# Kernel tuning notes

Hardware: AMD Instinct MI355X
Metric: run time of the kernel (lower is better)

Reference implementation:

```python
import jax, jax.numpy as jnp
import numpy as np

HEADS = 8
DIM_HEAD = 64
SCALE = DIM_HEAD ** -0.5
QUERY_DIM = 512
CTX_DIM = 64
INNER = HEADS * DIM_HEAD  # 512
GATE_HID = 32


def setup_inputs() -> dict:
    key = jax.random.key(0)
    ks = jax.random.split(key, 11)
    B, N, M = 4, 2048, 2048
    s = lambda fan: 1.0 / np.sqrt(fan)
    return {
        "x": jax.random.normal(ks[0], (B, N, QUERY_DIM), dtype=jnp.float32),
        "context": jax.random.normal(ks[1], (B, M, CTX_DIM), dtype=jnp.float32),
        "Wq": jax.random.normal(ks[2], (QUERY_DIM, INNER), dtype=jnp.float32) * s(QUERY_DIM),
        "Wk": jax.random.normal(ks[3], (CTX_DIM, INNER), dtype=jnp.float32) * s(CTX_DIM),
        "Wv": jax.random.normal(ks[4], (CTX_DIM, INNER), dtype=jnp.float32) * s(CTX_DIM),
        "W1": jax.random.normal(ks[5], (CTX_DIM, GATE_HID), dtype=jnp.float32) * s(CTX_DIM),
        "b1": jnp.zeros((GATE_HID,), dtype=jnp.float32),
        "W2": jax.random.normal(ks[6], (GATE_HID, 1), dtype=jnp.float32) * s(GATE_HID),
        "b2": jnp.zeros((1,), dtype=jnp.float32),
        "Wo": jax.random.normal(ks[7], (INNER, QUERY_DIM), dtype=jnp.float32) * s(INNER),
        "bo": jnp.zeros((QUERY_DIM,), dtype=jnp.float32),
    }


def reference(x, context, Wq, Wk, Wv, W1, b1, W2, b2, Wo, bo):
    B, N, _ = x.shape
    M = context.shape[1]
    # visual reliability gate: sigmoid(relu(ctx @ W1 + b1) @ W2 + b2) -> [B, M, 1]
    gate = jax.nn.sigmoid(jax.nn.relu(context @ W1 + b1) @ W2 + b2)
    ctx = context * gate
    # projections
    q = (x @ Wq).reshape(B, N, HEADS, DIM_HEAD).transpose(0, 2, 1, 3)    # [B,H,N,D]
    k = (ctx @ Wk).reshape(B, M, HEADS, DIM_HEAD).transpose(0, 2, 1, 3)  # [B,H,M,D]
    v = (ctx @ Wv).reshape(B, M, HEADS, DIM_HEAD).transpose(0, 2, 1, 3)  # [B,H,M,D]
    # scaled dot-product attention (full score matrix, as in source)
    sim = jnp.einsum('bhid,bhjd->bhij', q, k) * SCALE
    attn = jax.nn.softmax(sim, axis=-1)
    out = jnp.einsum('bhij,bhjd->bhid', attn, v)
    out = out.transpose(0, 2, 1, 3).reshape(B, N, INNER)
    return out @ Wo + bo
```

## Files before the change

### kernel.cpp

```cpp
#include <hip/hip_runtime.h>

typedef unsigned short u16;
typedef unsigned int u32;
using frag16 = __attribute__((ext_vector_type(8))) short;
using facc   = __attribute__((ext_vector_type(4))) float;
using facc16 = __attribute__((ext_vector_type(16))) float;

#define DEV static __device__ __forceinline__

DEV u16 f2bf(float f) {
  union { float f; unsigned u; } v; v.f = f;
  unsigned r = v.u + 0x7fffu + ((v.u >> 16) & 1u);
  return (u16)(r >> 16);
}
DEV unsigned fbits(float f) {
  union { float f; unsigned u; } v; v.f = f;
  return v.u;
}
DEV unsigned pkbf(float lo, float hi) {
  return __builtin_amdgcn_perm(fbits(hi) + 0x8000u, fbits(lo) + 0x8000u, 0x07060302u);
}
DEV void gld16(const u16* g, u16* l) {
  __builtin_amdgcn_global_load_lds(
      (__attribute__((address_space(1))) unsigned int*)(g),
      (__attribute__((address_space(3))) unsigned int*)(l), 16, 0, 0);
}

__global__ __launch_bounds__(256) void prep_gate_kernel(const float4* __restrict__ x,
    const float* __restrict__ Wq, const float* __restrict__ Wk,
    const float* __restrict__ Wv, const float* __restrict__ Wo,
    const float* __restrict__ ctx, const float* __restrict__ W1,
    const float* __restrict__ b1, const float* __restrict__ W2,
    const float* __restrict__ b2,
    u16* __restrict__ xb, u16* __restrict__ WqT, u16* __restrict__ WkT,
    u16* __restrict__ WvT, u16* __restrict__ WoT, u16* __restrict__ gctx) {
  int bid = blockIdx.x;
  if (bid < 4096) {
    int id = bid * 256 + threadIdx.x;
    float4 v = x[id];
    ushort4 o;
    o.x = f2bf(v.x); o.y = f2bf(v.y); o.z = f2bf(v.z); o.w = f2bf(v.w);
    *(ushort4*)(xb + (size_t)id * 4) = o;
  } else if (bid < 6400) {
    int id = (bid - 4096) * 256 + threadIdx.x;
    const float* W; u16* WT; int K, idx;
    if (id < 262144)      { W = Wq; WT = WqT; K = 512; idx = id; }
    else if (id < 294912) { W = Wk; WT = WkT; K = 64;  idx = id - 262144; }
    else if (id < 327680) { W = Wv; WT = WvT; K = 64;  idx = id - 294912; }
    else                  { W = Wo; WT = WoT; K = 512; idx = id - 327680; }
    int n = idx / K, k = idx - n * K;
    WT[idx] = f2bf(W[k * 512 + n]);
  } else {
    int wave = threadIdx.x >> 6, lane = threadIdx.x & 63;
    int row = (bid - 6400) * 4 + wave;
    __shared__ float sc[4][64];
    float cv = ctx[(size_t)row * 64 + lane];
    sc[wave][lane] = cv;
    __syncthreads();
    float h = 0.f;
    if (lane < 32) {
      h = b1[lane];
      #pragma unroll
      for (int i = 0; i < 64; ++i) h += sc[wave][i] * W1[i * 32 + lane];
      h = fmaxf(h, 0.f) * W2[lane];
    }
    #pragma unroll
    for (int off = 32; off; off >>= 1) h += __shfl_xor(h, off);
    float g = 1.f / (1.f + __expf(-(h + b2[0])));
    gctx[(size_t)row * 64 + lane] = f2bf(cv * g);
  }
}

template<int MODE>
DEV void gemm128_body(const u16* __restrict__ A, const u16* __restrict__ BT,
                      void* __restrict__ Cp, const float* __restrict__ bias,
                      int m0, int n0, float scale,
                      u16* As0, u16* As1, u16* Bs0, u16* Bs1) {
  const int K = 512, N = 512;
  const int lane = threadIdx.x & 63, wave = threadIdx.x >> 6;
  const int quad = lane >> 4, l16 = lane & 15;
  const int wr = wave >> 1, wc = wave & 1;

  const u16* gA = A + (size_t)(m0 + wave * 32 + (lane >> 2)) * K + (lane & 3) * 8;
  const u16* gB = BT + (size_t)(n0 + wave * 16 + (lane >> 2)) * K + (lane & 3) * 8;

  facc acc[4][2] = {};

  for (int k0 = 0; k0 < K; k0 += 64) {
    if (k0) __syncthreads();
    gld16(gA + k0,           As0 + wave * 1024);
    gld16(gA + 16 * K + k0,  As0 + wave * 1024 + 512);
    gld16(gA + k0 + 32,          As1 + wave * 1024);
    gld16(gA + 16 * K + k0 + 32, As1 + wave * 1024 + 512);
    gld16(gB + k0,      Bs0 + wave * 512);
    gld16(gB + k0 + 32, Bs1 + wave * 512);
    __syncthreads();

    #pragma unroll
    for (int hh = 0; hh < 2; ++hh) {
      const u16* Ah = hh ? As1 : As0;
      const u16* Bh = hh ? Bs1 : Bs0;
      frag16 af[4], bf[2];
      #pragma unroll
      for (int rt = 0; rt < 4; ++rt)
        af[rt] = *(const frag16*)(Ah + (wr * 64 + rt * 16 + l16) * 32 + quad * 8);
      #pragma unroll
      for (int ct = 0; ct < 2; ++ct)
        bf[ct] = *(const frag16*)(Bh + (wc * 32 + ct * 16 + l16) * 32 + quad * 8);
      #pragma unroll
      for (int rt = 0; rt < 4; ++rt)
        #pragma unroll
        for (int ct = 0; ct < 2; ++ct)
          acc[rt][ct] = __builtin_amdgcn_mfma_f32_16x16x32_bf16(af[rt], bf[ct], acc[rt][ct], 0, 0, 0);
    }
  }

  #pragma unroll
  for (int rt = 0; rt < 4; ++rt) {
    #pragma unroll
    for (int ct = 0; ct < 2; ++ct) {
      int col = n0 + wc * 32 + ct * 16 + l16;
      int r0g = m0 + wr * 64 + rt * 16 + quad * 4;
      if (MODE == 0) {
        u16* C = (u16*)Cp;
        #pragma unroll
        for (int r = 0; r < 4; ++r)
          C[(size_t)(r0g + r) * N + col] = f2bf(acc[rt][ct][r] * scale);
      } else {
        float* C = (float*)Cp;
        float bv = bias[col];
        #pragma unroll
        for (int r = 0; r < 4; ++r)
          C[(size_t)(r0g + r) * N + col] = acc[rt][ct][r] + bv;
      }
    }
  }
}

__global__ __launch_bounds__(256) void proj_kernel(const u16* __restrict__ xb,
    const u16* __restrict__ WqT, u16* __restrict__ qb,
    const u16* __restrict__ gctx, const u16* __restrict__ BkT,
    const u16* __restrict__ BvT, u16* __restrict__ Kp, u16* __restrict__ Vp) {
  __shared__ __align__(16) u16 As0[128 * 32], As1[128 * 32];
  __shared__ __align__(16) u16 Bs0[64 * 32], Bs1[64 * 32];
  int bid = blockIdx.x;
  if (bid < 512) {
    int n0 = (bid & 7) * 64, m0 = (bid >> 3) * 128;
    gemm128_body<0>(xb, WqT, qb, nullptr, m0, n0,
                    0.125f * 1.4426950408889634f, As0, As1, Bs0, Bs1);
    return;
  }
  bid -= 512;
  const int Kd = 64;
  int lane = threadIdx.x & 63, wave = threadIdx.x >> 6;
  int quad = lane >> 4, l16 = lane & 15;
  int wr = wave >> 1, wc = wave & 1;
  int rowBase = (bid >> 3) * 64 + wr * 32;
  int colBase = (bid & 7) * 64 + wc * 32;
  facc ak[2][2] = {}, av[2][2] = {};
  const u16* a0 = gctx + (size_t)(rowBase + l16) * Kd + quad * 8;
  const u16* a1 = a0 + (size_t)16 * Kd;
  const u16* bk0 = BkT + (size_t)(colBase + l16) * Kd + quad * 8;
  const u16* bk1 = bk0 + (size_t)16 * Kd;
  const u16* bv0 = BvT + (size_t)(colBase + l16) * Kd + quad * 8;
  const u16* bv1 = bv0 + (size_t)16 * Kd;
  #pragma unroll
  for (int kk = 0; kk < Kd; kk += 32) {
    frag16 af0 = *(const frag16*)(a0 + kk);
    frag16 af1 = *(const frag16*)(a1 + kk);
    frag16 k0 = *(const frag16*)(bk0 + kk);
    frag16 k1 = *(const frag16*)(bk1 + kk);
    frag16 v0 = *(const frag16*)(bv0 + kk);
    frag16 v1 = *(const frag16*)(bv1 + kk);
    ak[0][0] = __builtin_amdgcn_mfma_f32_16x16x32_bf16(af0, k0, ak[0][0], 0, 0, 0);
    ak[0][1] = __builtin_amdgcn_mfma_f32_16x16x32_bf16(af0, k1, ak[0][1], 0, 0, 0);
    ak[1][0] = __builtin_amdgcn_mfma_f32_16x16x32_bf16(af1, k0, ak[1][0], 0, 0, 0);
    ak[1][1] = __builtin_amdgcn_mfma_f32_16x16x32_bf16(af1, k1, ak[1][1], 0, 0, 0);
    av[0][0] = __builtin_amdgcn_mfma_f32_16x16x32_bf16(af0, v0, av[0][0], 0, 0, 0);
    av[0][1] = __builtin_amdgcn_mfma_f32_16x16x32_bf16(af0, v1, av[0][1], 0, 0, 0);
    av[1][0] = __builtin_amdgcn_mfma_f32_16x16x32_bf16(af1, v0, av[1][0], 0, 0, 0);
    av[1][1] = __builtin_amdgcn_mfma_f32_16x16x32_bf16(af1, v1, av[1][1], 0, 0, 0);
  }
  #pragma unroll
  for (int rt = 0; rt < 2; ++rt) {
    #pragma unroll
    for (int ct = 0; ct < 2; ++ct) {
      int col = colBase + ct * 16 + l16;
      int r0g = rowBase + rt * 16 + quad * 4;
      int hh = col >> 6, d = col & 63;
      int b = r0g >> 11;
      #pragma unroll
      for (int r = 0; r < 4; ++r) {
        int m = (r0g + r) & 2047;
        size_t addr = ((((size_t)(b * 8 + hh) * 64 + (m >> 5)) * 4 + (d >> 4)) * 64
                       + ((d >> 3) & 1) * 32 + (m & 31)) * 8 + (d & 7);
        Kp[addr] = f2bf(ak[rt][ct][r]);
      }
      int m = r0g & 2047;
      size_t addr = ((((size_t)(b * 8 + hh) * 64 + (m >> 5)) * 4
                      + ((m >> 4) & 1) * 2 + (d >> 5)) * 64
                     + ((m >> 3) & 1) * 32 + (d & 31)) * 8 + (m & 7);
      ushort4 o;
      o.x = f2bf(av[rt][ct][0]); o.y = f2bf(av[rt][ct][1]);
      o.z = f2bf(av[rt][ct][2]); o.w = f2bf(av[rt][ct][3]);
      *(ushort4*)(Vp + addr) = o;
    }
  }
}

__global__ __launch_bounds__(256, 3) void attn_kernel(
    const u16* __restrict__ qb, const u16* __restrict__ Kp,
    const u16* __restrict__ Vp, float* __restrict__ Opart,
    float* __restrict__ Lpart) {
  const int lane = threadIdx.x & 63, wave = threadIdx.x >> 6;
  const int l32 = lane & 31;
  const int hi = lane >> 5;
  const int bid = blockIdx.x;
  const int bh = bid & 31;
  const int qblk = (bid >> 5) & 15;
  const int js = bid >> 9;
  const int b = bh >> 3, h = bh & 7;
  const int q0 = (qblk * 4 + wave) * 32;
  const int rowg = b * 2048 + q0 + l32;

  __shared__ __align__(16) u16 sK[2][2048], sV[2][2048];

  const u16* qp = qb + (size_t)rowg * 512 + h * 64 + hi * 8;
  frag16 qf0 = *(const frag16*)(qp);
  frag16 qf1 = *(const frag16*)(qp + 16);
  frag16 qf2 = *(const frag16*)(qp + 32);
  frag16 qf3 = *(const frag16*)(qp + 48);

  facc16 O0 = {}, O1 = {};
  float lsum = 0.f;

  const size_t ts = 2048;
  const u16* kpb = Kp + (size_t)(bh * 64 + js * 32) * ts + wave * 512 + lane * 8;
  const u16* vpb = Vp + (size_t)(bh * 64 + js * 32) * ts + wave * 512 + lane * 8;

  gld16(kpb, sK[0] + wave * 512);
  gld16(vpb, sV[0] + wave * 512);

  for (int t = 0; t < 32; ++t) {
    const int p = t & 1;
    __syncthreads();
    if (t + 1 < 32) {
      gld16(kpb + (size_t)(t + 1) * ts, sK[p ^ 1] + wave * 512);
      gld16(vpb + (size_t)(t + 1) * ts, sV[p ^ 1] + wave * 512);
    }

    frag16 kf[4], vf[4];
    #pragma unroll
    for (int i = 0; i < 4; ++i) {
      kf[i] = *(const frag16*)(sK[p] + i * 512 + lane * 8);
      vf[i] = *(const frag16*)(sV[p] + i * 512 + lane * 8);
    }

    facc16 S = {};
    S = __builtin_amdgcn_mfma_f32_32x32x16_bf16(kf[0], qf0, S, 0, 0, 0);
    S = __builtin_amdgcn_mfma_f32_32x32x16_bf16(kf[1], qf1, S, 0, 0, 0);
    S = __builtin_amdgcn_mfma_f32_32x32x16_bf16(kf[2], qf2, S, 0, 0, 0);
    S = __builtin_amdgcn_mfma_f32_32x32x16_bf16(kf[3], qf3, S, 0, 0, 0);

    float e[16];
    #pragma unroll
    for (int r = 0; r < 16; ++r) e[r] = __builtin_amdgcn_exp2f(S[r]);
    #pragma unroll
    for (int r = 0; r < 16; ++r) lsum += e[r];

    unsigned pu[2][4];
    #pragma unroll
    for (int c = 0; c < 2; ++c) {
      const float* ee = e + c * 8;
      unsigned L0 = pkbf(ee[0], ee[1]);
      unsigned L1 = pkbf(ee[2], ee[3]);
      unsigned H0 = pkbf(ee[4], ee[5]);
      unsigned H1 = pkbf(ee[6], ee[7]);
      unsigned Y0 = hi ? L0 : H0;
      unsigned Y1 = hi ? L1 : H1;
      unsigned X0 = (unsigned)__shfl_xor((int)Y0, 32);
      unsigned X1 = (unsigned)__shfl_xor((int)Y1, 32);
      pu[c][0] = hi ? X0 : L0;
      pu[c][1] = hi ? X1 : L1;
      pu[c][2] = hi ? H0 : X0;
      pu[c][3] = hi ? H1 : X1;
    }
    frag16 P0 = *(frag16*)&pu[0][0];
    frag16 P1 = *(frag16*)&pu[1][0];

    O0 = __builtin_amdgcn_mfma_f32_32x32x16_bf16(vf[0], P0, O0, 0, 0, 0);
    O0 = __builtin_amdgcn_mfma_f32_32x32x16_bf16(vf[2], P1, O0, 0, 0, 0);
    O1 = __builtin_amdgcn_mfma_f32_32x32x16_bf16(vf[1], P0, O1, 0, 0, 0);
    O1 = __builtin_amdgcn_mfma_f32_32x32x16_bf16(vf[3], P1, O1, 0, 0, 0);
  }

  lsum += __shfl_xor(lsum, 32);

  float* op = Opart + ((size_t)js * 8192 + rowg) * 512 + h * 64;
  #pragma unroll
  for (int dt = 0; dt < 2; ++dt) {
    #pragma unroll
    for (int rq = 0; rq < 4; ++rq) {
      float4 v;
      if (dt == 0) { v.x = O0[rq*4]; v.y = O0[rq*4+1]; v.z = O0[rq*4+2]; v.w = O0[rq*4+3]; }
      else         { v.x = O1[rq*4]; v.y = O1[rq*4+1]; v.z = O1[rq*4+2]; v.w = O1[rq*4+3]; }
      int d0 = dt * 32 + 8 * rq + 4 * hi;
      *(float4*)(op + d0) = v;
    }
  }
  if (!hi) Lpart[(size_t)js * 65536 + (size_t)rowg * 8 + h] = lsum;
}

__global__ __launch_bounds__(256) void combine_kernel(const float* __restrict__ Opart,
    const float* __restrict__ Lpart, u16* __restrict__ ob) {
  int id = blockIdx.x * 256 + threadIdx.x;
  int row = id >> 7, c4 = (id & 127) * 4;
  int hh = c4 >> 6;
  size_t o = (size_t)row * 512 + c4;
  const float4 o0 = *(const float4*)(Opart + o);
  const float4 o1 = *(const float4*)(Opart + (size_t)8192 * 512 + o);
  float rl = 1.f / (Lpart[(size_t)row * 8 + hh] + Lpart[65536 + (size_t)row * 8 + hh]);
  ushort4 u;
  u.x = f2bf((o0.x + o1.x) * rl);
  u.y = f2bf((o0.y + o1.y) * rl);
  u.z = f2bf((o0.z + o1.z) * rl);
  u.w = f2bf((o0.w + o1.w) * rl);
  *(ushort4*)(ob + o) = u;
}

__global__ __launch_bounds__(256) void gemm_out(const u16* __restrict__ A,
    const u16* __restrict__ BT, float* __restrict__ C,
    const float* __restrict__ bias) {
  __shared__ __align__(16) u16 As0[128 * 32], As1[128 * 32];
  __shared__ __align__(16) u16 Bs0[64 * 32], Bs1[64 * 32];
  int n0 = (blockIdx.x & 7) * 64, m0 = (blockIdx.x >> 3) * 128;
  gemm128_body<2>(A, BT, C, bias, m0, n0, 1.f, As0, As1, Bs0, Bs1);
}

extern "C" void kernel_launch(void* const* d_in, const int* in_sizes, int n_in,
                              void* d_out, int out_size, void* d_ws, size_t ws_size,
                              hipStream_t stream) {
  const float* x   = (const float*)d_in[0];
  const float* ctx = (const float*)d_in[1];
  const float* Wq  = (const float*)d_in[2];
  const float* Wk  = (const float*)d_in[3];
  const float* Wv  = (const float*)d_in[4];
  const float* W1  = (const float*)d_in[5];
  const float* b1  = (const float*)d_in[6];
  const float* W2  = (const float*)d_in[7];
  const float* b2  = (const float*)d_in[8];
  const float* Wo  = (const float*)d_in[9];
  const float* bo  = (const float*)d_in[10];
  float* out = (float*)d_out;

  char* ws = (char*)d_ws;
  size_t off = 0;
  auto alloc = [&](size_t bytes) {
    char* p = ws + off;
    off += (bytes + 255) & ~(size_t)255;
    return p;
  };
  u16* xb    = (u16*)alloc(8192ull * 512 * 2);
  u16* qb    = (u16*)alloc(8192ull * 512 * 2);
  u16* Kp    = (u16*)alloc(8192ull * 512 * 2);
  u16* Vp    = (u16*)alloc(8192ull * 512 * 2);
  u16* ob    = (u16*)alloc(8192ull * 512 * 2);
  u16* gctx  = (u16*)alloc(8192ull * 64 * 2);
  u16* WqT   = (u16*)alloc(512ull * 512 * 2);
  u16* WkT   = (u16*)alloc(512ull * 64 * 2);
  u16* WvT   = (u16*)alloc(512ull * 64 * 2);
  u16* WoT   = (u16*)alloc(512ull * 512 * 2);
  float* Opart = (float*)alloc(2ull * 8192 * 512 * 4);
  float* Lpart = (float*)alloc(2ull * 65536 * 4);

  prep_gate_kernel<<<8448, 256, 0, stream>>>((const float4*)x, Wq, Wk, Wv, Wo,
                                             ctx, W1, b1, W2, b2,
                                             xb, WqT, WkT, WvT, WoT, gctx);
  proj_kernel<<<1536, 256, 0, stream>>>(xb, WqT, qb, gctx, WkT, WvT, Kp, Vp);
  attn_kernel<<<1024, 256, 0, stream>>>(qb, Kp, Vp, Opart, Lpart);
  combine_kernel<<<4096, 256, 0, stream>>>(Opart, Lpart, ob);
  gemm_out<<<512, 256, 0, stream>>>(ob, WoT, out, bo);
}
```

Baseline: 181.6 us.

## Drop split-KV attention and combine kernel; process two KV tiles per iteration

The attention kernel no longer splits the key dimension across two blocks. Each block now walks all 64 KV tiles, two per iteration with doubled LDS buffers, and normalizes and writes bf16 output directly. This removes the fp32 partial buffers, the extra combine launch, and their global memory traffic, and halves the barrier count per tile. In exchange the grid halves to 512 blocks, LDS per block doubles, and launch bounds drop to 2 blocks per CU, which may leave CUs underfilled.

Result: faster. 172.2 us (-5.1%).

```diff
diff --git a/kernel.cpp b/kernel.cpp
--- a/kernel.cpp
+++ b/kernel.cpp
@@ -208,22 +208,20 @@
   }
 }
 
-__global__ __launch_bounds__(256, 3) void attn_kernel(
+__global__ __launch_bounds__(256, 2) void attn_kernel(
     const u16* __restrict__ qb, const u16* __restrict__ Kp,
-    const u16* __restrict__ Vp, float* __restrict__ Opart,
-    float* __restrict__ Lpart) {
+    const u16* __restrict__ Vp, u16* __restrict__ ob) {
   const int lane = threadIdx.x & 63, wave = threadIdx.x >> 6;
   const int l32 = lane & 31;
   const int hi = lane >> 5;
   const int bid = blockIdx.x;
   const int bh = bid & 31;
-  const int qblk = (bid >> 5) & 15;
-  const int js = bid >> 9;
+  const int qblk = bid >> 5;
   const int b = bh >> 3, h = bh & 7;
   const int q0 = (qblk * 4 + wave) * 32;
   const int rowg = b * 2048 + q0 + l32;
 
-  __shared__ __align__(16) u16 sK[2][2048], sV[2][2048];
+  __shared__ __align__(16) u16 sK[2][2][2048], sV[2][2][2048];
 
   const u16* qp = qb + (size_t)rowg * 512 + h * 64 + hi * 8;
   frag16 qf0 = *(const frag16*)(qp);
@@ -235,97 +233,123 @@
   float lsum = 0.f;
 
   const size_t ts = 2048;
-  const u16* kpb = Kp + (size_t)(bh * 64 + js * 32) * ts + wave * 512 + lane * 8;
-  const u16* vpb = Vp + (size_t)(bh * 64 + js * 32) * ts + wave * 512 + lane * 8;
-
-  gld16(kpb, sK[0] + wave * 512);
-  gld16(vpb, sV[0] + wave * 512);
-
-  for (int t = 0; t < 32; ++t) {
-    const int p = t & 1;
+  const u16* kpb = Kp + (size_t)(bh * 64) * ts + wave * 512 + lane * 8;
+  const u16* vpb = Vp + (size_t)(bh * 64) * ts + wave * 512 + lane * 8;
+
+  gld16(kpb,      sK[0][0] + wave * 512);
+  gld16(kpb + ts, sK[0][1] + wave * 512);
+  gld16(vpb,      sV[0][0] + wave * 512);
+  gld16(vpb + ts, sV[0][1] + wave * 512);
+
+  for (int g = 0; g < 32; ++g) {
+    const int p = g & 1;
     __syncthreads();
-    if (t + 1 < 32) {
-      gld16(kpb + (size_t)(t + 1) * ts, sK[p ^ 1] + wave * 512);
-      gld16(vpb + (size_t)(t + 1) * ts, sV[p ^ 1] + wave * 512);
-    }
-
-    frag16 kf[4], vf[4];
+    if (g + 1 < 32) {
+      const size_t t2 = (size_t)(2 * g + 2) * ts;
+      gld16(kpb + t2,      sK[p ^ 1][0] + wave * 512);
+      gld16(kpb + t2 + ts, sK[p ^ 1][1] + wave * 512);
+      gld16(vpb + t2,      sV[p ^ 1][0] + wave * 512);
+      gld16(vpb + t2 + ts, sV[p ^ 1][1] + wave * 512);
+    }
+
+    frag16 kfa[4], kfb[4];
     #pragma unroll
     for (int i = 0; i < 4; ++i) {
-      kf[i] = *(const frag16*)(sK[p] + i * 512 + lane * 8);
-      vf[i] = *(const frag16*)(sV[p] + i * 512 + lane * 8);
-    }
-
-    facc16 S = {};
-    S = __builtin_amdgcn_mfma_f32_32x32x16_bf16(kf[0], qf0, S, 0, 0, 0);
-    S = __builtin_amdgcn_mfma_f32_32x32x16_bf16(kf[1], qf1, S, 0, 0, 0);
-    S = __builtin_amdgcn_mfma_f32_32x32x16_bf16(kf[2], qf2, S, 0, 0, 0);
-    S = __builtin_amdgcn_mfma_f32_32x32x16_bf16(kf[3], qf3, S, 0, 0, 0);
-
-    float e[16];
-    #pragma unroll
-    for (int r = 0; r < 16; ++r) e[r] = __builtin_amdgcn_exp2f(S[r]);
-    #pragma unroll
-    for (int r = 0; r < 16; ++r) lsum += e[r];
-
-    unsigned pu[2][4];
+      kfa[i] = *(const frag16*)(sK[p][0] + i * 512 + lane * 8);
+      kfb[i] = *(const frag16*)(sK[p][1] + i * 512 + lane * 8);
+    }
+
+    facc16 Sa = {}, Sb = {};
+    Sa = __builtin_amdgcn_mfma_f32_32x32x16_bf16(kfa[0], qf0, Sa, 0, 0, 0);
+    Sb = __builtin_amdgcn_mfma_f32_32x32x16_bf16(kfb[0], qf0, Sb, 0, 0, 0);
+    Sa = __builtin_amdgcn_mfma_f32_32x32x16_bf16(kfa[1], qf1, Sa, 0, 0, 0);
+    Sb = __builtin_amdgcn_mfma_f32_32x32x16_bf16(kfb[1], qf1, Sb, 0, 0, 0);
+    Sa = __builtin_amdgcn_mfma_f32_32x32x16_bf16(kfa[2], qf2, Sa, 0, 0, 0);
+    Sb = __builtin_amdgcn_mfma_f32_32x32x16_bf16(kfb[2], qf2, Sb, 0, 0, 0);
+    Sa = __builtin_amdgcn_mfma_f32_32x32x16_bf16(kfa[3], qf3, Sa, 0, 0, 0);
+    Sb = __builtin_amdgcn_mfma_f32_32x32x16_bf16(kfb[3], qf3, Sb, 0, 0, 0);
+
+    float ea[16], eb[16];
+    #pragma unroll
+    for (int r = 0; r < 16; ++r) { ea[r] = __builtin_amdgcn_exp2f(Sa[r]);
+                                   eb[r] = __builtin_amdgcn_exp2f(Sb[r]); }
+    #pragma unroll
+    for (int r = 0; r < 16; ++r) lsum += ea[r] + eb[r];
+
+    unsigned pua[2][4], pub[2][4];
     #pragma unroll
     for (int c = 0; c < 2; ++c) {
-      const float* ee = e + c * 8;
-      unsigned L0 = pkbf(ee[0], ee[1]);
-      unsigned L1 = pkbf(ee[2], ee[3]);
-      unsigned H0 = pkbf(ee[4], ee[5]);
-      unsigned H1 = pkbf(ee[6], ee[7]);
-      unsigned Y0 = hi ? L0 : H0;
-      unsigned Y1 = hi ? L1 : H1;
-      unsigned X0 = (unsigned)__shfl_xor((int)Y0, 32);
-      unsigned X1 = (unsigned)__shfl_xor((int)Y1, 32);
-      pu[c][0] = hi ? X0 : L0;
-      pu[c][1] = hi ? X1 : L1;
-      pu[c][2] = hi ? H0 : X0;
-      pu[c][3] = hi ? H1 : X1;
-    }
-    frag16 P0 = *(frag16*)&pu[0][0];
-    frag16 P1 = *(frag16*)&pu[1][0];
-
-    O0 = __builtin_amdgcn_mfma_f32_32x32x16_bf16(vf[0], P0, O0, 0, 0, 0);
-    O0 = __builtin_amdgcn_mfma_f32_32x32x16_bf16(vf[2], P1, O0, 0, 0, 0);
-    O1 = __builtin_amdgcn_mfma_f32_32x32x16_bf16(vf[1], P0, O1, 0, 0, 0);
-    O1 = __builtin_amdgcn_mfma_f32_32x32x16_bf16(vf[3], P1, O1, 0, 0, 0);
+      {
+        const float* ee = ea + c * 8;
+        unsigned L0 = pkbf(ee[0], ee[1]);
+        unsigned L1 = pkbf(ee[2], ee[3]);
+        unsigned H0 = pkbf(ee[4], ee[5]);
+        unsigned H1 = pkbf(ee[6], ee[7]);
+        unsigned Y0 = hi ? L0 : H0;
+        unsigned Y1 = hi ? L1 : H1;
+        unsigned X0 = (unsigned)__shfl_xor((int)Y0, 32);
+        unsigned X1 = (unsigned)__shfl_xor((int)Y1, 32);
+        pua[c][0] = hi ? X0 : L0;
+        pua[c][1] = hi ? X1 : L1;
+        pua[c][2] = hi ? H0 : X0;
+        pua[c][3] = hi ? H1 : X1;
+      }
+      {
+        const float* ee = eb + c * 8;
+        unsigned L0 = pkbf(ee[0], ee[1]);
+        unsigned L1 = pkbf(ee[2], ee[3]);
+        unsigned H0 = pkbf(ee[4], ee[5]);
+        unsigned H1 = pkbf(ee[6], ee[7]);
+        unsigned Y0 = hi ? L0 : H0;
+        unsigned Y1 = hi ? L1 : H1;
+        unsigned X0 = (unsigned)__shfl_xor((int)Y0, 32);
+        unsigned X1 = (unsigned)__shfl_xor((int)Y1, 32);
+        pub[c][0] = hi ? X0 : L0;
+        pub[c][1] = hi ? X1 : L1;
+        pub[c][2] = hi ? H0 : X0;
+        pub[c][3] = hi ? H1 : X1;
+      }
+    }
+    frag16 Pa0 = *(frag16*)&pua[0][0];
+    frag16 Pa1 = *(frag16*)&pua[1][0];
+    frag16 Pb0 = *(frag16*)&pub[0][0];
+    frag16 Pb1 = *(frag16*)&pub[1][0];
+
+    frag16 vfa[4], vfb[4];
+    #pragma unroll
+    for (int i = 0; i < 4; ++i) {
+      vfa[i] = *(const frag16*)(sV[p][0] + i * 512 + lane * 8);
+      vfb[i] = *(const frag16*)(sV[p][1] + i * 512 + lane * 8);
+    }
+
+    O0 = __builtin_amdgcn_mfma_f32_32x32x16_bf16(vfa[0], Pa0, O0, 0, 0, 0);
+    O1 = __builtin_amdgcn_mfma_f32_32x32x16_bf16(vfa[1], Pa0, O1, 0, 0, 0);
+    O0 = __builtin_amdgcn_mfma_f32_32x32x16_bf16(vfa[2], Pa1, O0, 0, 0, 0);
+    O1 = __builtin_amdgcn_mfma_f32_32x32x16_bf16(vfa[3], Pa1, O1, 0, 0, 0);
+    O0 = __builtin_amdgcn_mfma_f32_32x32x16_bf16(vfb[0], Pb0, O0, 0, 0, 0);
+    O1 = __builtin_amdgcn_mfma_f32_32x32x16_bf16(vfb[1], Pb0, O1, 0, 0, 0);
+    O0 = __builtin_amdgcn_mfma_f32_32x32x16_bf16(vfb[2], Pb1, O0, 0, 0, 0);
+    O1 = __builtin_amdgcn_mfma_f32_32x32x16_bf16(vfb[3], Pb1, O1, 0, 0, 0);
   }
 
   lsum += __shfl_xor(lsum, 32);
-
-  float* op = Opart + ((size_t)js * 8192 + rowg) * 512 + h * 64;
+  float rinv = 1.0f / lsum;
+
+  u16* op = ob + (size_t)rowg * 512 + h * 64;
   #pragma unroll
   for (int dt = 0; dt < 2; ++dt) {
     #pragma unroll
     for (int rq = 0; rq < 4; ++rq) {
-      float4 v;
-      if (dt == 0) { v.x = O0[rq*4]; v.y = O0[rq*4+1]; v.z = O0[rq*4+2]; v.w = O0[rq*4+3]; }
-      else         { v.x = O1[rq*4]; v.y = O1[rq*4+1]; v.z = O1[rq*4+2]; v.w = O1[rq*4+3]; }
+      float v0, v1, v2, v3;
+      if (dt == 0) { v0 = O0[rq*4]; v1 = O0[rq*4+1]; v2 = O0[rq*4+2]; v3 = O0[rq*4+3]; }
+      else         { v0 = O1[rq*4]; v1 = O1[rq*4+1]; v2 = O1[rq*4+2]; v3 = O1[rq*4+3]; }
+      uint2 pk;
+      pk.x = pkbf(v0 * rinv, v1 * rinv);
+      pk.y = pkbf(v2 * rinv, v3 * rinv);
       int d0 = dt * 32 + 8 * rq + 4 * hi;
-      *(float4*)(op + d0) = v;
-    }
-  }
-  if (!hi) Lpart[(size_t)js * 65536 + (size_t)rowg * 8 + h] = lsum;
-}
-
-__global__ __launch_bounds__(256) void combine_kernel(const float* __restrict__ Opart,
-    const float* __restrict__ Lpart, u16* __restrict__ ob) {
-  int id = blockIdx.x * 256 + threadIdx.x;
-  int row = id >> 7, c4 = (id & 127) * 4;
-  int hh = c4 >> 6;
-  size_t o = (size_t)row * 512 + c4;
-  const float4 o0 = *(const float4*)(Opart + o);
-  const float4 o1 = *(const float4*)(Opart + (size_t)8192 * 512 + o);
-  float rl = 1.f / (Lpart[(size_t)row * 8 + hh] + Lpart[65536 + (size_t)row * 8 + hh]);
-  ushort4 u;
-  u.x = f2bf((o0.x + o1.x) * rl);
-  u.y = f2bf((o0.y + o1.y) * rl);
-  u.z = f2bf((o0.z + o1.z) * rl);
-  u.w = f2bf((o0.w + o1.w) * rl);
-  *(ushort4*)(ob + o) = u;
+      *(uint2*)(op + d0) = pk;
+    }
+  }
 }
 
 __global__ __launch_bounds__(256) void gemm_out(const u16* __restrict__ A,
@@ -370,14 +394,11 @@
   u16* WkT   = (u16*)alloc(512ull * 64 * 2);
   u16* WvT   = (u16*)alloc(512ull * 64 * 2);
   u16* WoT   = (u16*)alloc(512ull * 512 * 2);
-  float* Opart = (float*)alloc(2ull * 8192 * 512 * 4);
-  float* Lpart = (float*)alloc(2ull * 65536 * 4);
 
   prep_gate_kernel<<<8448, 256, 0, stream>>>((const float4*)x, Wq, Wk, Wv, Wo,
                                              ctx, W1, b1, W2, b2,
                                              xb, WqT, WkT, WvT, WoT, gctx);
   proj_kernel<<<1536, 256, 0, stream>>>(xb, WqT, qb, gctx, WkT, WvT, Kp, Vp);
-  attn_kernel<<<1024, 256, 0, stream>>>(qb, Kp, Vp, Opart, Lpart);
-  combine_kernel<<<4096, 256, 0, stream>>>(Opart, Lpart, ob);
+  attn_kernel<<<512, 256, 0, stream>>>(qb, Kp, Vp, ob);
   gemm_out<<<512, 256, 0, stream>>>(ob, WoT, out, bo);
 }
```
